# Performance work log

Measured on AMD Instinct MI355X. Metric: run time of the kernel, lower is better.

The kernel has to match this reference:

```python
import jax, jax.numpy as jnp
import numpy as np

# CapsuleConv2d(128, 256, 3, in_length=16, out_length=16, stride=1, padding=1,
#               share_weight=True, routing_type='k_means' (dot), num_iterations=3, squash=True)
KH = KW = 3
SH = SW = 1
PH = PW = 1
DH = DW = 1
IN_LENGTH = 16
OUT_LENGTH = 16
NUM_ITERS = 3
EPS = 1e-12


def _extract_patches(x):
    # x: [B, C, H, W] -> [B, C, KH, KW, OH, OW] (torch.nn.functional.unfold layout)
    B, C, H, W = x.shape
    OH = (H + 2 * PH - DH * (KH - 1) - 1) // SH + 1
    OW = (W + 2 * PW - DW * (KW - 1) - 1) // SW + 1
    xp = jnp.pad(x, ((0, 0), (0, 0), (PH, PH), (PW, PW)))
    rows = []
    for i in range(KH):  # small fixed kernel loop
        cols = []
        for j in range(KW):
            cols.append(xp[:, :, i * DH: i * DH + (OH - 1) * SH + 1: SH,
                              j * DW: j * DW + (OW - 1) * SW + 1: SW])
        rows.append(jnp.stack(cols, axis=2))
    return jnp.stack(rows, axis=2)  # [B, C, KH, KW, OH, OW]


def _k_means_routing(u, num_iterations):
    # u: [B, OH, OW, N_in, O, L]; routing over N_in (axis -3), dot similarity
    v = u.mean(axis=-3, keepdims=True)  # [B, OH, OW, 1, O, L]
    for _ in range(num_iterations):
        vn = v / jnp.maximum(jnp.linalg.norm(v, axis=-1, keepdims=True), EPS)
        logits = jnp.sum(u * vn, axis=-1, keepdims=True)      # [B,OH,OW,N_in,O,1]
        probs = jax.nn.softmax(logits, axis=-3)
        v = jnp.sum(probs * u, axis=-3, keepdims=True)
    return jnp.squeeze(v, axis=-3)  # [B, OH, OW, O, L]


def _squash(s):
    norm = jnp.linalg.norm(s, axis=-1, keepdims=True)
    return s * (norm / (1.0 + norm * norm))  # = ||s||^2/(1+||s||^2) * s/||s||


def setup_inputs() -> dict:
    key = jax.random.key(0)
    k1, k2 = jax.random.split(key)
    x = jax.random.normal(k1, (2, 128, 32, 32), dtype=jnp.float32)
    # weight: [O=out_channels//out_length, L=out_length, M=in_length, KH, KW]
    fan = IN_LENGTH * KH * KW + OUT_LENGTH * KH * KW
    bound = float(np.sqrt(6.0 / fan))  # xavier_uniform-ish scale
    weight = jax.random.uniform(k2, (16, 16, 16, 3, 3), dtype=jnp.float32,
                                minval=-bound, maxval=bound)
    return {"x": x, "weight": weight}


def reference(x, weight):
    B = x.shape[0]
    O, L, M = weight.shape[0], weight.shape[1], weight.shape[2]
    patches = _extract_patches(x)                      # [B, C, KH, KW, OH, OW]
    OH, OW = patches.shape[-2], patches.shape[-1]
    G = x.shape[1] // M
    patches = patches.reshape(B, G, M, KH, KW, OH, OW)
    # priors[b,h,w,g,i,j,o,l] = sum_m patch[b,g,m,i,j,h,w] * weight[o,l,m,i,j]
    priors = jnp.einsum('bgmijhw,olmij->bhwgijol', patches, weight)
    priors = priors.reshape(B, OH, OW, G * KH * KW, O, L)
    v = _k_means_routing(priors, NUM_ITERS)            # [B, OH, OW, O, L]
    v = _squash(v)
    out = v.reshape(B, OH, OW, O * L).transpose(0, 3, 1, 2)  # [B, C_out, OH, OW]
    return out
```

## Files before the change

### kernel.cpp

```cpp
#include <hip/hip_runtime.h>


typedef float v2f __attribute__((ext_vector_type(2)));
typedef int   i4  __attribute__((ext_vector_type(4)));
typedef short bh8 __attribute__((ext_vector_type(8)));
typedef float f16v __attribute__((ext_vector_type(16)));

#define STR 34

#define DPP_ADD(a, ctrl)                                                     \
  a += __int_as_float(__builtin_amdgcn_update_dpp(                           \
          0, __float_as_int(a), ctrl, 0xF, 0xF, true))

__device__ __forceinline__ float dpp_add16(float x) {
    float s = x;
    DPP_ADD(s, 0x128); DPP_ADD(s, 0x124); DPP_ADD(s, 0x122); DPP_ADD(s, 0x121);
    return s;
}

__device__ __forceinline__ float swz16_add(float x) {
    int y = __builtin_amdgcn_ds_swizzle(__float_as_int(x), 0x401F);
    return x + __int_as_float(y);
}

__device__ __forceinline__ float frcp(float x) {
    return __builtin_amdgcn_rcpf(x);
}

__device__ __forceinline__ v2f pkfma(v2f a, v2f b, v2f c) {
    return __builtin_elementwise_fma(a, b, c);
}

#define BFRAG(BH, BL, IJ) {                                                  \
    float q0 = uLds[wb + (IJ)];                                              \
    float q1 = uLds[wb + (IJ) + 9];                                          \
    float q2 = uLds[wb + (IJ) + 18];                                         \
    float q3 = uLds[wb + (IJ) + 27];                                         \
    float q4 = uLds[wb + (IJ) + 36];                                         \
    float q5 = uLds[wb + (IJ) + 45];                                         \
    float q6 = uLds[wb + (IJ) + 54];                                         \
    float q7 = uLds[wb + (IJ) + 63];                                         \
    unsigned d0 = __float_as_uint(q0), d1 = __float_as_uint(q1);             \
    unsigned d2 = __float_as_uint(q2), d3 = __float_as_uint(q3);             \
    unsigned d4 = __float_as_uint(q4), d5 = __float_as_uint(q5);             \
    unsigned d6 = __float_as_uint(q6), d7 = __float_as_uint(q7);             \
    BH.x = (int)((d0 >> 16) | (d1 & 0xFFFF0000u));                           \
    BH.y = (int)((d2 >> 16) | (d3 & 0xFFFF0000u));                           \
    BH.z = (int)((d4 >> 16) | (d5 & 0xFFFF0000u));                           \
    BH.w = (int)((d6 >> 16) | (d7 & 0xFFFF0000u));                           \
    unsigned e0 = __float_as_uint(q0 - __uint_as_float(d0 & 0xFFFF0000u));   \
    unsigned e1 = __float_as_uint(q1 - __uint_as_float(d1 & 0xFFFF0000u));   \
    unsigned e2 = __float_as_uint(q2 - __uint_as_float(d2 & 0xFFFF0000u));   \
    unsigned e3 = __float_as_uint(q3 - __uint_as_float(d3 & 0xFFFF0000u));   \
    unsigned e4 = __float_as_uint(q4 - __uint_as_float(d4 & 0xFFFF0000u));   \
    unsigned e5 = __float_as_uint(q5 - __uint_as_float(d5 & 0xFFFF0000u));   \
    unsigned e6 = __float_as_uint(q6 - __uint_as_float(d6 & 0xFFFF0000u));   \
    unsigned e7 = __float_as_uint(q7 - __uint_as_float(d7 & 0xFFFF0000u));   \
    BL.x = (int)((e0 >> 16) | (e1 & 0xFFFF0000u));                           \
    BL.y = (int)((e2 >> 16) | (e3 & 0xFFFF0000u));                           \
    BL.z = (int)((e4 >> 16) | (e5 & 0xFFFF0000u));                           \
    BL.w = (int)((e6 >> 16) | (e7 & 0xFFFF0000u)); }

#define CWR(REG, IJ)                                                         \
    uLds[wroff + STR * ((((REG) >> 2) * 72) + (((REG) & 3) * 9) + (IJ))] =   \
        acc[(REG)];

#define DO_IJ(IJ, BH, BL)                                                    \
  { const int di = (IJ) / 3, dj = (IJ) % 3;                                  \
    const int hh = h + di - 1;                                               \
    const bool hok = (unsigned)hh < 32u;                                     \
    const int hhc = hok ? hh : 0;                                            \
    const int ww = w0 + pl + dj - 1;                                         \
    const bool ok = hok && ((unsigned)ww < 32u);                             \
    const int wwc = ok ? ww : 0;                                             \
    const float* ap = x + bb * 131072 + (gl * 16 + half * 8) * 1024          \
                        + hhc * 32 + wwc;                                    \
    float f0 = ap[0],    f1 = ap[1024], f2 = ap[2048], f3 = ap[3072];        \
    float f4 = ap[4096], f5 = ap[5120], f6 = ap[6144], f7 = ap[7168];        \
    const float msk = ok ? 1.0f : 0.0f;                                      \
    f0 *= msk; f1 *= msk; f2 *= msk; f3 *= msk;                              \
    f4 *= msk; f5 *= msk; f6 *= msk; f7 *= msk;                              \
    unsigned b0 = __float_as_uint(f0), b1 = __float_as_uint(f1);             \
    unsigned b2 = __float_as_uint(f2), b3 = __float_as_uint(f3);             \
    unsigned b4 = __float_as_uint(f4), b5 = __float_as_uint(f5);             \
    unsigned b6 = __float_as_uint(f6), b7 = __float_as_uint(f7);             \
    i4 hp, lp;                                                               \
    hp.x = (int)((b0 >> 16) | (b1 & 0xFFFF0000u));                           \
    hp.y = (int)((b2 >> 16) | (b3 & 0xFFFF0000u));                           \
    hp.z = (int)((b4 >> 16) | (b5 & 0xFFFF0000u));                           \
    hp.w = (int)((b6 >> 16) | (b7 & 0xFFFF0000u));                           \
    unsigned l0 = __float_as_uint(f0 - __uint_as_float(b0 & 0xFFFF0000u));   \
    unsigned l1 = __float_as_uint(f1 - __uint_as_float(b1 & 0xFFFF0000u));   \
    unsigned l2 = __float_as_uint(f2 - __uint_as_float(b2 & 0xFFFF0000u));   \
    unsigned l3 = __float_as_uint(f3 - __uint_as_float(b3 & 0xFFFF0000u));   \
    unsigned l4 = __float_as_uint(f4 - __uint_as_float(b4 & 0xFFFF0000u));   \
    unsigned l5 = __float_as_uint(f5 - __uint_as_float(b5 & 0xFFFF0000u));   \
    unsigned l6 = __float_as_uint(f6 - __uint_as_float(b6 & 0xFFFF0000u));   \
    unsigned l7 = __float_as_uint(f7 - __uint_as_float(b7 & 0xFFFF0000u));   \
    lp.x = (int)((l0 >> 16) | (l1 & 0xFFFF0000u));                           \
    lp.y = (int)((l2 >> 16) | (l3 & 0xFFFF0000u));                           \
    lp.z = (int)((l4 >> 16) | (l5 & 0xFFFF0000u));                           \
    lp.w = (int)((l6 >> 16) | (l7 & 0xFFFF0000u));                           \
    bh8 aHi = __builtin_bit_cast(bh8, hp);                                   \
    bh8 aLo = __builtin_bit_cast(bh8, lp);                                   \
    bh8 bHi = __builtin_bit_cast(bh8, BH);                                   \
    bh8 bLo = __builtin_bit_cast(bh8, BL);                                   \
    f16v acc = {0.f,0.f,0.f,0.f,0.f,0.f,0.f,0.f,                             \
                0.f,0.f,0.f,0.f,0.f,0.f,0.f,0.f};                            \
    acc = __builtin_amdgcn_mfma_f32_32x32x16_bf16(aHi, bLo, acc, 0, 0, 0);   \
    acc = __builtin_amdgcn_mfma_f32_32x32x16_bf16(aLo, bHi, acc, 0, 0, 0);   \
    acc = __builtin_amdgcn_mfma_f32_32x32x16_bf16(aHi, bHi, acc, 0, 0, 0);   \
    CWR(0, IJ)  CWR(1, IJ)  CWR(2, IJ)  CWR(3, IJ)                           \
    CWR(4, IJ)  CWR(5, IJ)  CWR(6, IJ)  CWR(7, IJ)                           \
    CWR(8, IJ)  CWR(9, IJ)  CWR(10, IJ) CWR(11, IJ)                          \
    CWR(12, IJ) CWR(13, IJ) CWR(14, IJ) CWR(15, IJ) }

#define LROW(K)                                                              \
  { const v2f* r2_ = (const v2f*)(rb + (K) * 16 * STR);                      \
    U##K##0 = r2_[0]; U##K##1 = r2_[1]; U##K##2 = r2_[2]; U##K##3 = r2_[3]; }

#define DOTR(K)                                                              \
  ({ v2f d_ = U##K##0 * V0;                                                  \
     d_ = pkfma(U##K##1, V1, d_); d_ = pkfma(U##K##2, V2, d_);               \
     d_ = pkfma(U##K##3, V3, d_); swz16_add(d_.x + d_.y); })

#define MEANJ(J)                                                             \
  { v2f s_ = (U0##J + U1##J) + (U2##J + U3##J) + U4##J;                      \
    V##J.x = dpp_add16(s_.x) * (1.0f / 72.0f);                               \
    V##J.y = dpp_add16(s_.y) * (1.0f / 72.0f); }

#define UPDJ(J)                                                              \
  { v2f pv_ = e0v * U0##J;                                                   \
    pv_ = pkfma(e1v, U1##J, pv_); pv_ = pkfma(e2v, U2##J, pv_);              \
    pv_ = pkfma(e3v, U3##J, pv_); pv_ = pkfma(e4v, U4##J, pv_);              \
    V##J.x = dpp_add16(pv_.x) * rs;                                          \
    V##J.y = dpp_add16(pv_.y) * rs; }

__global__ __launch_bounds__(256, 4)
void capsule_v10(const float* __restrict__ x, const float* __restrict__ W,
                 float* __restrict__ out) {
    __shared__ float uLds[4 * 72 * STR];
    const int blk = blockIdx.x;
    const int tt = blk & 7;
    const int q  = blk >> 3;
    const int bb = q >> 8;
    const int r  = q & 255;
    const int h  = r >> 3;
    const int w0 = (r & 7) << 2;
    const int tid = threadIdx.x;

    {
        const float* gw = W + tt * 4608;
        #pragma unroll
        for (int rr = 0; rr < 18; ++rr) {
            int i = rr * 256 + tid;
            uLds[i + (i / 144)] = gw[i];
        }
    }
    __syncthreads();

    {
        const int lane = tid & 63;
        const int wv   = tid >> 6;
        const int pl   = (lane & 31) >> 3;
        const int gl   = lane & 7;
        const int half = lane >> 5;
        const int tl   = lane & 31;
        const int wroff = tl + STR * 9 * 4 * half;
        const int wb = (lane & 31) * 145 + (lane >> 5) * 72;

        i4 B0h = {0,0,0,0}, B0l = {0,0,0,0};
        i4 B1h = {0,0,0,0}, B1l = {0,0,0,0};
        i4 B2h = {0,0,0,0}, B2l = {0,0,0,0};
        if (wv == 0)      { BFRAG(B0h,B0l,0) BFRAG(B1h,B1l,4) BFRAG(B2h,B2l,8) }
        else if (wv == 1) { BFRAG(B0h,B0l,1) BFRAG(B1h,B1l,5) }
        else if (wv == 2) { BFRAG(B0h,B0l,2) BFRAG(B1h,B1l,6) }
        else              { BFRAG(B0h,B0l,3) BFRAG(B1h,B1l,7) }
        __syncthreads();

        if (wv == 0)      { DO_IJ(0,B0h,B0l) DO_IJ(4,B1h,B1l) DO_IJ(8,B2h,B2l) }
        else if (wv == 1) { DO_IJ(1,B0h,B0l) DO_IJ(5,B1h,B1l) }
        else if (wv == 2) { DO_IJ(2,B0h,B0l) DO_IJ(6,B1h,B1l) }
        else              { DO_IJ(3,B0h,B0l) DO_IJ(7,B1h,B1l) }
    }
    __syncthreads();

    const int p  = tid >> 6;
    const int i6 = tid & 63;
    const int o2 = i6 >> 5;
    const int jh = (i6 >> 4) & 1;
    const int sc = i6 & 15;
    const bool has5 = (sc < 8);
    const float* rb = uLds + (p * 72 + sc) * STR + o2 * 16 + jh * 8;

    v2f U00, U01, U02, U03;
    v2f U10, U11, U12, U13;
    v2f U20, U21, U22, U23;
    v2f U30, U31, U32, U33;
    v2f U40, U41, U42, U43;
    U40 = U41 = U42 = U43 = (v2f){0.0f, 0.0f};
    LROW(0) LROW(1) LROW(2) LROW(3)
    if (has5) LROW(4)

    v2f V0, V1, V2, V3;
    MEANJ(0) MEANJ(1) MEANJ(2) MEANJ(3)

    #pragma unroll 1
    for (int it = 0; it < 3; ++it) {
        v2f ssv = V0 * V0;
        ssv = pkfma(V1, V1, ssv); ssv = pkfma(V2, V2, ssv);
        ssv = pkfma(V3, V3, ssv);
        float ss = swz16_add(ssv.x + ssv.y);
        float inv = frcp(fmaxf(sqrtf(ss), 1e-12f));

        float E0 = __expf(DOTR(0) * inv);
        float E1 = __expf(DOTR(1) * inv);
        float E2 = __expf(DOTR(2) * inv);
        float E3 = __expf(DOTR(3) * inv);
        float E4 = has5 ? __expf(DOTR(4) * inv) : 0.0f;
        float ssum = dpp_add16(((E0 + E1) + (E2 + E3)) + E4);
        float rs = frcp(ssum);

        v2f e0v = {E0, E0}, e1v = {E1, E1}, e2v = {E2, E2};
        v2f e3v = {E3, E3}, e4v = {E4, E4};
        UPDJ(0) UPDJ(1) UPDJ(2) UPDJ(3)
    }

    v2f ssv = V0 * V0;
    ssv = pkfma(V1, V1, ssv); ssv = pkfma(V2, V2, ssv);
    ssv = pkfma(V3, V3, ssv);
    float ss = swz16_add(ssv.x + ssv.y);
    float scale = sqrtf(ss) * frcp(1.0f + ss);

    v2f aa0 = (sc & 4) ? V2 : V0;
    v2f aa1 = (sc & 4) ? V3 : V1;
    v2f bb0 = (sc & 2) ? aa1 : aa0;
    float res = ((sc & 1) ? bb0.y : bb0.x) * scale;
    if (sc < 8) {
        int tg = tt * 32 + o2 * 16 + jh * 8 + sc;
        out[((bb * 256 + tg) * 32 + h) * 32 + w0 + p] = res;
    }
}

extern "C" void kernel_launch(void* const* d_in, const int* in_sizes, int n_in,
                              void* d_out, int out_size, void* d_ws, size_t ws_size,
                              hipStream_t stream) {
    const float* x = (const float*)d_in[0];
    const float* W = (const float*)d_in[1];
    float* out = (float*)d_out;
    (void)d_ws; (void)ws_size; (void)in_sizes; (void)n_in; (void)out_size;
    capsule_v10<<<4096, 256, 0, stream>>>(x, W, out);
}
```

Before: 86.94 us.

## Process four pixel quads per block, reusing weight fragments held in registers

Each block now handles 16 output pixels (four quads of 4) instead of 4, looping over the quads with the weight B-fragments kept in registers. The weights are loaded straight from global memory into the MFMA fragments, skipping the LDS staging pass and one barrier. The grid shrinks from 4096 to 1024 blocks, which cuts repeated weight loading and conversion per block. In exchange each block runs longer, there are fewer blocks to spread across the CUs, and each quad iteration adds two barriers.

```diff
diff --git a/kernel.cpp b/kernel.cpp
--- a/kernel.cpp
+++ b/kernel.cpp
@@ -31,15 +31,10 @@
     return __builtin_elementwise_fma(a, b, c);
 }
 
-#define BFRAG(BH, BL, IJ) {                                                  \
-    float q0 = uLds[wb + (IJ)];                                              \
-    float q1 = uLds[wb + (IJ) + 9];                                          \
-    float q2 = uLds[wb + (IJ) + 18];                                         \
-    float q3 = uLds[wb + (IJ) + 27];                                         \
-    float q4 = uLds[wb + (IJ) + 36];                                         \
-    float q5 = uLds[wb + (IJ) + 45];                                         \
-    float q6 = uLds[wb + (IJ) + 54];                                         \
-    float q7 = uLds[wb + (IJ) + 63];                                         \
+#define BFRAGG(BH, BL, IJ) {                                                 \
+    const float* wp_ = Wg + (IJ);                                            \
+    float q0 = wp_[0],  q1 = wp_[9],  q2 = wp_[18], q3 = wp_[27];            \
+    float q4 = wp_[36], q5 = wp_[45], q6 = wp_[54], q7 = wp_[63];            \
     unsigned d0 = __float_as_uint(q0), d1 = __float_as_uint(q1);             \
     unsigned d2 = __float_as_uint(q2), d3 = __float_as_uint(q3);             \
     unsigned d4 = __float_as_uint(q4), d5 = __float_as_uint(q5);             \
@@ -61,25 +56,26 @@
     BL.z = (int)((e4 >> 16) | (e5 & 0xFFFF0000u));                           \
     BL.w = (int)((e6 >> 16) | (e7 & 0xFFFF0000u)); }
 
-#define CWR(REG, IJ)                                                         \
-    uLds[wroff + STR * ((((REG) >> 2) * 72) + (((REG) & 3) * 9) + (IJ))] =   \
-        acc[(REG)];
-
-#define DO_IJ(IJ, BH, BL)                                                    \
-  { const int di = (IJ) / 3, dj = (IJ) % 3;                                  \
+#define ALOAD(A, M, IJ) {                                                    \
+    const int di = (IJ) / 3, dj = (IJ) % 3;                                  \
     const int hh = h + di - 1;                                               \
     const bool hok = (unsigned)hh < 32u;                                     \
     const int hhc = hok ? hh : 0;                                            \
     const int ww = w0 + pl + dj - 1;                                         \
     const bool ok = hok && ((unsigned)ww < 32u);                             \
     const int wwc = ok ? ww : 0;                                             \
-    const float* ap = x + bb * 131072 + (gl * 16 + half * 8) * 1024          \
-                        + hhc * 32 + wwc;                                    \
-    float f0 = ap[0],    f1 = ap[1024], f2 = ap[2048], f3 = ap[3072];        \
-    float f4 = ap[4096], f5 = ap[5120], f6 = ap[6144], f7 = ap[7168];        \
-    const float msk = ok ? 1.0f : 0.0f;                                      \
-    f0 *= msk; f1 *= msk; f2 *= msk; f3 *= msk;                              \
-    f4 *= msk; f5 *= msk; f6 *= msk; f7 *= msk;                              \
+    const float* ap = xq + hhc * 32 + wwc;                                   \
+    M = ok ? 1.0f : 0.0f;                                                    \
+    A[0] = ap[0];    A[1] = ap[1024]; A[2] = ap[2048]; A[3] = ap[3072];      \
+    A[4] = ap[4096]; A[5] = ap[5120]; A[6] = ap[6144]; A[7] = ap[7168]; }
+
+#define CWR(REG, IJ)                                                         \
+    uLds[wroff + STR * ((((REG) >> 2) * 72) + (((REG) & 3) * 9) + (IJ))] =   \
+        acc[(REG)];
+
+#define PACKMFMA(A, M, IJ, BH, BL) {                                         \
+    float f0 = A[0]*M, f1 = A[1]*M, f2 = A[2]*M, f3 = A[3]*M;                \
+    float f4 = A[4]*M, f5 = A[5]*M, f6 = A[6]*M, f7 = A[7]*M;                \
     unsigned b0 = __float_as_uint(f0), b1 = __float_as_uint(f1);             \
     unsigned b2 = __float_as_uint(f2), b3 = __float_as_uint(f3);             \
     unsigned b4 = __float_as_uint(f4), b5 = __float_as_uint(f5);             \
@@ -137,53 +133,34 @@
     V##J.y = dpp_add16(pv_.y) * rs; }
 
 __global__ __launch_bounds__(256, 4)
-void capsule_v10(const float* __restrict__ x, const float* __restrict__ W,
+void capsule_v11(const float* __restrict__ x, const float* __restrict__ W,
                  float* __restrict__ out) {
     __shared__ float uLds[4 * 72 * STR];
-    const int blk = blockIdx.x;
-    const int tt = blk & 7;
-    const int q  = blk >> 3;
-    const int bb = q >> 8;
-    const int r  = q & 255;
-    const int h  = r >> 3;
-    const int w0 = (r & 7) << 2;
-    const int tid = threadIdx.x;
-
-    {
-        const float* gw = W + tt * 4608;
-        #pragma unroll
-        for (int rr = 0; rr < 18; ++rr) {
-            int i = rr * 256 + tid;
-            uLds[i + (i / 144)] = gw[i];
-        }
-    }
-    __syncthreads();
-
-    {
-        const int lane = tid & 63;
-        const int wv   = tid >> 6;
-        const int pl   = (lane & 31) >> 3;
-        const int gl   = lane & 7;
-        const int half = lane >> 5;
-        const int tl   = lane & 31;
-        const int wroff = tl + STR * 9 * 4 * half;
-        const int wb = (lane & 31) * 145 + (lane >> 5) * 72;
-
-        i4 B0h = {0,0,0,0}, B0l = {0,0,0,0};
-        i4 B1h = {0,0,0,0}, B1l = {0,0,0,0};
-        i4 B2h = {0,0,0,0}, B2l = {0,0,0,0};
-        if (wv == 0)      { BFRAG(B0h,B0l,0) BFRAG(B1h,B1l,4) BFRAG(B2h,B2l,8) }
-        else if (wv == 1) { BFRAG(B0h,B0l,1) BFRAG(B1h,B1l,5) }
-        else if (wv == 2) { BFRAG(B0h,B0l,2) BFRAG(B1h,B1l,6) }
-        else              { BFRAG(B0h,B0l,3) BFRAG(B1h,B1l,7) }
-        __syncthreads();
-
-        if (wv == 0)      { DO_IJ(0,B0h,B0l) DO_IJ(4,B1h,B1l) DO_IJ(8,B2h,B2l) }
-        else if (wv == 1) { DO_IJ(1,B0h,B0l) DO_IJ(5,B1h,B1l) }
-        else if (wv == 2) { DO_IJ(2,B0h,B0l) DO_IJ(6,B1h,B1l) }
-        else              { DO_IJ(3,B0h,B0l) DO_IJ(7,B1h,B1l) }
-    }
-    __syncthreads();
+    const int blk  = blockIdx.x;
+    const int tt   = blk & 7;
+    const int rest = blk >> 3;
+    const int bb   = rest >> 6;
+    const int h    = (rest >> 1) & 31;
+    const int wh   = rest & 1;
+    const int tid  = threadIdx.x;
+
+    const int lane = tid & 63;
+    const int wv   = tid >> 6;
+    const int pl   = (lane & 31) >> 3;
+    const int gl   = lane & 7;
+    const int half = lane >> 5;
+    const int tl   = lane & 31;
+    const int wroff = tl + STR * 9 * 4 * half;
+    const float* xq = x + bb * 131072 + (gl * 16 + half * 8) * 1024;
+    const float* Wg = W + tt * 4608 + (lane & 31) * 144 + (lane >> 5) * 72;
+
+    i4 B0h = {0,0,0,0}, B0l = {0,0,0,0};
+    i4 B1h = {0,0,0,0}, B1l = {0,0,0,0};
+    i4 B2h = {0,0,0,0}, B2l = {0,0,0,0};
+    if (wv == 0)      { BFRAGG(B0h,B0l,0) BFRAGG(B1h,B1l,4) BFRAGG(B2h,B2l,8) }
+    else if (wv == 1) { BFRAGG(B0h,B0l,1) BFRAGG(B1h,B1l,5) }
+    else if (wv == 2) { BFRAGG(B0h,B0l,2) BFRAGG(B1h,B1l,6) }
+    else              { BFRAGG(B0h,B0l,3) BFRAGG(B1h,B1l,7) }
 
     const int p  = tid >> 6;
     const int i6 = tid & 63;
@@ -193,52 +170,82 @@
     const bool has5 = (sc < 8);
     const float* rb = uLds + (p * 72 + sc) * STR + o2 * 16 + jh * 8;
 
-    v2f U00, U01, U02, U03;
-    v2f U10, U11, U12, U13;
-    v2f U20, U21, U22, U23;
-    v2f U30, U31, U32, U33;
-    v2f U40, U41, U42, U43;
-    U40 = U41 = U42 = U43 = (v2f){0.0f, 0.0f};
-    LROW(0) LROW(1) LROW(2) LROW(3)
-    if (has5) LROW(4)
-
-    v2f V0, V1, V2, V3;
-    MEANJ(0) MEANJ(1) MEANJ(2) MEANJ(3)
-
     #pragma unroll 1
-    for (int it = 0; it < 3; ++it) {
+    for (int qi = 0; qi < 4; ++qi) {
+        const int w0 = wh * 16 + qi * 4;
+
+        {
+            float a0[8], a1[8], a2[8];
+            float m0, m1, m2;
+            if (wv == 0) {
+                ALOAD(a0, m0, 0) ALOAD(a1, m1, 4) ALOAD(a2, m2, 8)
+                PACKMFMA(a0, m0, 0, B0h, B0l)
+                PACKMFMA(a1, m1, 4, B1h, B1l)
+                PACKMFMA(a2, m2, 8, B2h, B2l)
+            } else if (wv == 1) {
+                ALOAD(a0, m0, 1) ALOAD(a1, m1, 5)
+                PACKMFMA(a0, m0, 1, B0h, B0l)
+                PACKMFMA(a1, m1, 5, B1h, B1l)
+            } else if (wv == 2) {
+                ALOAD(a0, m0, 2) ALOAD(a1, m1, 6)
+                PACKMFMA(a0, m0, 2, B0h, B0l)
+                PACKMFMA(a1, m1, 6, B1h, B1l)
+            } else {
+                ALOAD(a0, m0, 3) ALOAD(a1, m1, 7)
+                PACKMFMA(a0, m0, 3, B0h, B0l)
+                PACKMFMA(a1, m1, 7, B1h, B1l)
+            }
+        }
+        __syncthreads();
+
+        v2f U00, U01, U02, U03;
+        v2f U10, U11, U12, U13;
+        v2f U20, U21, U22, U23;
+        v2f U30, U31, U32, U33;
+        v2f U40, U41, U42, U43;
+        U40 = U41 = U42 = U43 = (v2f){0.0f, 0.0f};
+        LROW(0) LROW(1) LROW(2) LROW(3)
+        if (has5) LROW(4)
+        __syncthreads();
+
+        v2f V0, V1, V2, V3;
+        MEANJ(0) MEANJ(1) MEANJ(2) MEANJ(3)
+
+        #pragma unroll 1
+        for (int it = 0; it < 3; ++it) {
+            v2f ssv = V0 * V0;
+            ssv = pkfma(V1, V1, ssv); ssv = pkfma(V2, V2, ssv);
+            ssv = pkfma(V3, V3, ssv);
+            float ss = swz16_add(ssv.x + ssv.y);
+            float inv = frcp(fmaxf(sqrtf(ss), 1e-12f));
+
+            float E0 = __expf(DOTR(0) * inv);
+            float E1 = __expf(DOTR(1) * inv);
+            float E2 = __expf(DOTR(2) * inv);
+            float E3 = __expf(DOTR(3) * inv);
+            float E4 = has5 ? __expf(DOTR(4) * inv) : 0.0f;
+            float ssum = dpp_add16(((E0 + E1) + (E2 + E3)) + E4);
+            float rs = frcp(ssum);
+
+            v2f e0v = {E0, E0}, e1v = {E1, E1}, e2v = {E2, E2};
+            v2f e3v = {E3, E3}, e4v = {E4, E4};
+            UPDJ(0) UPDJ(1) UPDJ(2) UPDJ(3)
+        }
+
         v2f ssv = V0 * V0;
         ssv = pkfma(V1, V1, ssv); ssv = pkfma(V2, V2, ssv);
         ssv = pkfma(V3, V3, ssv);
         float ss = swz16_add(ssv.x + ssv.y);
-        float inv = frcp(fmaxf(sqrtf(ss), 1e-12f));
-
-        float E0 = __expf(DOTR(0) * inv);
-        float E1 = __expf(DOTR(1) * inv);
-        float E2 = __expf(DOTR(2) * inv);
-        float E3 = __expf(DOTR(3) * inv);
-        float E4 = has5 ? __expf(DOTR(4) * inv) : 0.0f;
-        float ssum = dpp_add16(((E0 + E1) + (E2 + E3)) + E4);
-        float rs = frcp(ssum);
-
-        v2f e0v = {E0, E0}, e1v = {E1, E1}, e2v = {E2, E2};
-        v2f e3v = {E3, E3}, e4v = {E4, E4};
-        UPDJ(0) UPDJ(1) UPDJ(2) UPDJ(3)
-    }
-
-    v2f ssv = V0 * V0;
-    ssv = pkfma(V1, V1, ssv); ssv = pkfma(V2, V2, ssv);
-    ssv = pkfma(V3, V3, ssv);
-    float ss = swz16_add(ssv.x + ssv.y);
-    float scale = sqrtf(ss) * frcp(1.0f + ss);
-
-    v2f aa0 = (sc & 4) ? V2 : V0;
-    v2f aa1 = (sc & 4) ? V3 : V1;
-    v2f bb0 = (sc & 2) ? aa1 : aa0;
-    float res = ((sc & 1) ? bb0.y : bb0.x) * scale;
-    if (sc < 8) {
-        int tg = tt * 32 + o2 * 16 + jh * 8 + sc;
-        out[((bb * 256 + tg) * 32 + h) * 32 + w0 + p] = res;
+        float scale = sqrtf(ss) * frcp(1.0f + ss);
+
+        v2f aa0 = (sc & 4) ? V2 : V0;
+        v2f aa1 = (sc & 4) ? V3 : V1;
+        v2f bb0 = (sc & 2) ? aa1 : aa0;
+        float res = ((sc & 1) ? bb0.y : bb0.x) * scale;
+        if (sc < 8) {
+            int tg = tt * 32 + o2 * 16 + jh * 8 + sc;
+            out[((bb * 256 + tg) * 32 + h) * 32 + w0 + p] = res;
+        }
     }
 }
 
@@ -249,5 +256,5 @@
     const float* W = (const float*)d_in[1];
     float* out = (float*)d_out;
     (void)d_ws; (void)ws_size; (void)in_sizes; (void)n_in; (void)out_size;
-    capsule_v10<<<4096, 256, 0, stream>>>(x, W, out);
-}
+    capsule_v11<<<1024, 256, 0, stream>>>(x, W, out);
+}
```

After: 91.41 us. +5.1%, slower.
